# Kernel optimization log

Hardware: AMD Instinct MI355X
Metric: run time of the kernel (lower is better)

Reference implementation:

```python
import jax, jax.numpy as jnp
import numpy as np

B, N_SIDE, S = 64, 40, 512
N = N_SIDE * N_SIDE          # 1600 grid points (fl_feature_dims [1,40,40])
EMB = 10                     # embedding_dim
GDIM = 8                     # lie('homography').dim
WIDTH = 128
C1 = 20                      # first-layer output channels


def _embed(x, emb_dim):
    # sinusoidal embedding of each scalar coordinate: [..., D] -> [..., D*emb_dim]
    freqs = 2.0 ** jnp.arange(emb_dim // 2, dtype=x.dtype)
    ang = x[..., None] * freqs                       # [..., D, emb/2]
    e = jnp.concatenate([jnp.sin(ang), jnp.cos(ang)], axis=-1)  # [..., D, emb]
    return e.reshape(x.shape[:-1] + (x.shape[-1] * emb_dim,))


def _glorot(key, shape):
    fan_in = shape[0]
    return jax.random.normal(key, shape, dtype=jnp.float32) / np.sqrt(fan_in)


def setup_inputs() -> dict:
    key = jax.random.key(0)
    ks = jax.random.split(key, 16)
    inp = {
        'data':   jax.random.normal(ks[0], (B, N, 1), dtype=jnp.float32),
        'v0':     jax.random.normal(ks[1], (S, GDIM), dtype=jnp.float32),
        'v_last': jax.random.normal(ks[2], (S, GDIM), dtype=jnp.float32),
        # FirstLayer filter MLP: 2*EMB -> 20 -> 20 -> 1*C1
        'fl_w1': _glorot(ks[3], (2 * EMB, 20)), 'fl_b1': jnp.zeros((20,), jnp.float32),
        'fl_w2': _glorot(ks[4], (20, 20)),      'fl_b2': jnp.zeros((20,), jnp.float32),
        'fl_w3': _glorot(ks[5], (20, C1)),      'fl_b3': jnp.zeros((C1,), jnp.float32),
        # Hidden FilterMLP: EMB*GDIM=80 -> WIDTH -> C1*WIDTH
        's_w1': _glorot(ks[6], (EMB * GDIM, WIDTH)), 's_b1': jnp.zeros((WIDTH,), jnp.float32),
        's_w2': _glorot(ks[7], (WIDTH, C1 * WIDTH)), 's_b2': jnp.zeros((C1 * WIDTH,), jnp.float32),
        'fc1_w': _glorot(ks[8], (WIDTH, WIDTH)), 'fc1_b': jnp.zeros((WIDTH,), jnp.float32),
        'fc2_w': _glorot(ks[9], (WIDTH, WIDTH)), 'fc2_b': jnp.zeros((WIDTH,), jnp.float32),
        'pool_w': _glorot(ks[10], (WIDTH, 10)),  'pool_b': jnp.zeros((10,), jnp.float32),
    }
    return inp


def reference(data, v0, v_last, fl_w1, fl_b1, fl_w2, fl_b2, fl_w3, fl_b3,
              s_w1, s_b1, s_w2, s_b2, fc1_w, fc1_b, fc2_w, fc2_b, pool_w, pool_b):
    silu = jax.nn.silu
    # pixel grid in [-1,1]^2, homogeneous coords [N,3]
    lin = jnp.linspace(-1.0, 1.0, N_SIDE, dtype=data.dtype)
    xx, yy = jnp.meshgrid(lin, lin, indexing='ij')
    coords = jnp.stack([xx.ravel(), yy.ravel()], axis=-1)           # [N,2]
    xh = jnp.concatenate([coords, jnp.ones((N, 1), data.dtype)], -1)  # [N,3]
    # homography matrices: identity + small perturbation from 8 group params
    pert = jnp.concatenate([0.1 * v_last, jnp.zeros((S, 1), data.dtype)], -1).reshape(S, 3, 3)
    H = jnp.eye(3, dtype=data.dtype) + pert                          # [S,3,3]
    y = jnp.einsum('sij,nj->sni', H, xh)                             # [S,N,3]
    t = y[..., :2] / y[..., 2:3]                                     # projective action [S,N,2]
    # continuous-kernel first layer: filters generated by MLP on embedded coords
    e1 = _embed(t, EMB)                                              # [S,N,20]
    h = silu(e1 @ fl_w1 + fl_b1)
    h = silu(h @ fl_w2 + fl_b2)
    filt1 = h @ fl_w3 + fl_b3                                        # [S,N,C1]
    z = jnp.einsum('bn,sno->bso', data[:, :, 0], filt1) / N          # [B,S,C1]
    z = silu(z)
    # hidden FilterMLP on group samples v0 -> per-sample filters [S,C1,WIDTH]
    v0e = _embed(v0, EMB)                                            # [S,80]
    h2 = silu(v0e @ s_w1 + s_b1)                                     # [S,WIDTH]
    filt2 = (h2 @ s_w2 + s_b2).reshape(S, C1, WIDTH)
    # (1/S) * sum over group-sample and channel axes of broadcast product
    z = jnp.einsum('bsc,scw->bw', z, filt2) / S                      # [B,WIDTH]
    z = silu(z @ fc1_w + fc1_b) + z
    z = silu(z @ fc2_w + fc2_b) + z
    return z @ pool_w + pool_b                                       # [B,10]
```

## Files before the change

### kernel.cpp

```cpp
#include <hip/hip_runtime.h>

#define N_PTS 1600
#define NSIDE 40
#define SNUM  512
#define BNUM  64
#define C1D   20
#define WID   128

typedef _Float16 h8  __attribute__((ext_vector_type(8)));
typedef _Float16 h4  __attribute__((ext_vector_type(4)));
typedef __fp16   h2v __attribute__((ext_vector_type(2)));
typedef float    f4  __attribute__((ext_vector_type(4)));

__device__ __forceinline__ float silu_f(float x){
    return x * __builtin_amdgcn_rcpf(1.f + __expf(-x));
}
__device__ __forceinline__ void fma4(float4& a, float s, const float4 w){
    a.x += s*w.x; a.y += s*w.y; a.z += s*w.z; a.w += s*w.w;
}

__device__ __forceinline__ void embed_coord(
    int n, float hA, float hB, float hC, float h6, float h7, float h8c,
    h2v e5[5])
{
    const int i = n / NSIDE;
    const int j = n - i * NSIDE;
    const float x = -1.f + (float)i * (2.f/39.f);
    const float y = -1.f + (float)j * (2.f/39.f);
    const float yc = hA*x + hB*y + hC;
    const float y2 = h6*x + h7*y + h8c;
    const float tc = yc * __builtin_amdgcn_rcpf(y2);
    float e[10];
    float sv, cv;
    __sincosf(tc, &sv, &cv);
    #pragma unroll
    for (int k = 0; k < 5; k++) {
        e[k] = sv; e[5+k] = cv;
        const float ns = 2.f*sv*cv, nc = 1.f - 2.f*sv*sv; sv = ns; cv = nc;
    }
    #pragma unroll
    for (int k = 0; k < 5; k++)
        e5[k] = __builtin_amdgcn_cvt_pkrtz(e[2*k], e[2*k+1]);
}

#define ASTRIDE 40

__global__ __launch_bounds__(512, 6) void kaf_fused(
    const float* __restrict__ data, const float* __restrict__ v0,
    const float* __restrict__ v_last,
    const float* __restrict__ s_w1, const float* __restrict__ s_b1,
    const float* __restrict__ s_w2, const float* __restrict__ s_b2,
    const float* __restrict__ w1, const float* __restrict__ b1,
    const float* __restrict__ w2, const float* __restrict__ b2,
    const float* __restrict__ w3, const float* __restrict__ b3,
    _Float16* __restrict__ dataA, float* __restrict__ f2g,
    float* __restrict__ out2g, _Float16* __restrict__ filtG)
{
    const int t  = threadIdx.x;
    const int bx = blockIdx.x;

    __shared__ __align__(16) unsigned char smem[27008];

    if (bx >= 1024) {
        if (bx == 1689) {
            for (int v = t; v < 8192; v += 512) out2g[v] = 0.f;
            return;
        }
        if (bx >= 1664) {
            const int o  = (bx - 1664) * 512 + t;
            const int L  = o & 63, cm = o >> 6;
            const int mt = cm & 3, ch = cm >> 2;
            const int b  = mt * 16 + (L & 15);
            const int nb = ch * 32 + (L >> 4) * 8;
            const float* src = data + b * N_PTS + nb;
            h8 v;
            #pragma unroll
            for (int j = 0; j < 8; j++) v[j] = (_Float16)src[j];
            *(h8*)(dataA + (size_t)o * 8) = v;
            return;
        }
        const int bxe = bx - 1024;
        const int st  = bxe / 10, ct = bxe - st * 10;
        const int s0  = st * 8;
        float* h2t = (float*)smem;
        float* svt = (float*)(smem + 6144);

        if (t < 64) {
            const int ss = t >> 3, d = t & 7;
            const float val = v0[(s0 + ss) * 8 + d];
            float sv, cv;
            __sincosf(val, &sv, &cv);
            #pragma unroll
            for (int k = 0; k < 5; k++) {
                svt[(ss*8 + d)*10 + k]     = sv;
                svt[(ss*8 + d)*10 + 5 + k] = cv;
                const float ns = 2.f * sv * cv;
                const float nc = 1.f - 2.f * sv * sv;
                sv = ns; cv = nc;
            }
        }
        __syncthreads();

        {
            const int j  = t & 127;
            const int sh = t >> 7;
            const float bias1 = s_b1[j];
            float h0 = bias1, h1 = bias1;
            for (int d = 0; d < 8; d++) {
                #pragma unroll
                for (int kk = 0; kk < 10; kk++) {
                    const float wv = s_w1[(d * 10 + kk) * WID + j];
                    h0 += svt[((sh*2    )*8 + d)*10 + kk] * wv;
                    h1 += svt[((sh*2 + 1)*8 + d)*10 + kk] * wv;
                }
            }
            h2t[j*12 + sh*2    ] = silu_f(h0);
            h2t[j*12 + sh*2 + 1] = silu_f(h1);
        }
        __syncthreads();

        const int col = ct * 256 + (t & 255);
        const int g   = t >> 8;
        float4 acc = make_float4(0.f, 0.f, 0.f, 0.f);
        #pragma unroll 4
        for (int i = 0; i < 128; i++) {
            const float wv = s_w2[i * 2560 + col];
            const float4 hh = *(const float4*)&h2t[i*12 + g*4];
            fma4(acc, wv, hh);
        }
        const float bias = s_b2[col];
        const float* af = (const float*)&acc;
        #pragma unroll
        for (int u = 0; u < 4; u++)
            f2g[(s0 + g*4 + u) * 2560 + col] = af[u] + bias;
        return;
    }

    const int s    = bx & 511;
    const int half = bx >> 9;
    const int nb0  = half * 800;
    const int lane = t & 63;
    const int w    = t >> 6;
    const int q    = lane >> 4;
    const int l15  = lane & 15;
    const int ep   = lane >> 1;
    const int ec   = lane & 1;
    const int erow = w*16 + ep + ((ep >> 4) * 112);

    _Float16* act  = (_Float16*)smem;
    _Float16* wlds = (_Float16*)(smem + 20480);
    float*    blds = (float*)   (smem + 26624);

    {
        const float* wsrc[3] = { w1, w2, w3 };
        const float* bsrc[3] = { b1, b2, b3 };
        for (int v = t; v < 3072; v += 512) {
            const int l = v >> 10, rem = v & 1023;
            const int cout = rem >> 5, cin = rem & 31;
            float x = 0.f;
            if (cout < 20 && cin < 20) x = wsrc[l][cin * 20 + cout];
            wlds[v] = (_Float16)x;
        }
        if (t < 96) {
            const int l = t >> 5, cout = t & 31;
            blds[t] = (cout < 20) ? bsrc[l][cout] : 0.f;
        }
    }

    float Hm[9];
    #pragma unroll
    for (int k = 0; k < 9; k++) Hm[k] = (k == 0 || k == 4 || k == 8) ? 1.f : 0.f;
    #pragma unroll
    for (int k = 0; k < 8; k++) Hm[k] += 0.1f * v_last[s*8 + k];
    const float hA = ec ? Hm[3] : Hm[0];
    const float hB = ec ? Hm[4] : Hm[1];
    const float hC = ec ? Hm[5] : Hm[2];

    if (ec == 0) {
        unsigned long long* pz = (unsigned long long*)(act + erow*ASTRIDE + 20);
        pz[0] = 0ull; pz[1] = 0ull; pz[2] = 0ull;
    }

    __syncthreads();

    _Float16* fgs = filtG + (size_t)(half*512 + s) * 16000;

    for (int base = 0; base < 800; base += 256) {
        const int tn = min(256, 800 - base);

        if (erow < tn) {
            h2v e5[5];
            embed_coord(nb0 + base + erow, hA, hB, hC, Hm[6], Hm[7], Hm[8], e5);
            #pragma unroll
            for (int k = 0; k < 5; k++)
                *(h2v*)(act + erow*ASTRIDE + ec*10 + 2*k) = e5[k];
        }

        const int nmt = tn >> 4;
        #pragma unroll
        for (int l = 0; l < 3; l++) {
            const h8 wf0 = *(const h8*)(wlds + ((l*2+0)*16 + l15) * 32 + q*8);
            const h8 wf1 = *(const h8*)(wlds + ((l*2+1)*16 + l15) * 32 + q*8);
            const float b0 = blds[(l*2+0)*16 + l15];
            const float b1 = blds[(l*2+1)*16 + l15];
            const f4 zero4 = (f4)(0.f);
            for (int mt = w; mt < nmt; mt += 8) {
                const int r0 = mt * 16;
                const h8 af = *(const h8*)(act + (r0 + l15)*ASTRIDE + q*8);
                f4 D0 = __builtin_amdgcn_mfma_f32_16x16x32_f16(af, wf0, zero4, 0, 0, 0);
                f4 D1 = __builtin_amdgcn_mfma_f32_16x16x32_f16(af, wf1, zero4, 0, 0, 0);
                if (l < 2) {
                    #pragma unroll
                    for (int r = 0; r < 4; r++) {
                        const int p = r0 + q*4 + r;
                        act[p*ASTRIDE + l15] = (_Float16)silu_f(D0[r] + b0);
                        if (l15 < 4)
                            act[p*ASTRIDE + 16 + l15] = (_Float16)silu_f(D1[r] + b1);
                    }
                } else {
                    h4 p0, p1;
                    #pragma unroll
                    for (int r = 0; r < 4; r++) {
                        p0[r] = (_Float16)(D0[r] + b0);
                        p1[r] = (_Float16)(D1[r] + b1);
                    }
                    *(h4*)(fgs + l15*800 + base + r0 + q*4) = p0;
                    if (l15 < 4)
                        *(h4*)(fgs + (16 + l15)*800 + base + r0 + q*4) = p1;
                }
            }
        }
    }
}

__global__ __launch_bounds__(256, 6) void kz_gemm(
    const _Float16* __restrict__ dataA, const _Float16* __restrict__ filtG,
    float* __restrict__ zpart)
{
    const int s    = blockIdx.x & 511;
    const int half = blockIdx.x >> 9;
    const int t    = threadIdx.x;
    const int lane = t & 63;
    const int w    = t >> 6;
    const int q    = lane >> 4;
    const int l15  = lane & 15;

    __shared__ __align__(16) float red[4 * 64 * 21];

    const _Float16* fgs = filtG + (size_t)(half*512 + s) * 16000;
    const int r1row = (l15 < 4) ? (16 + l15) : 0;

    f4 zacc[4][2];
    #pragma unroll
    for (int mt = 0; mt < 4; mt++) { zacc[mt][0] = (f4)(0.f); zacc[mt][1] = (f4)(0.f); }

    #pragma unroll 2
    for (int kc = w; kc < 25; kc += 4) {
        const h8 bf0 = *(const h8*)(fgs + l15  *800 + kc*32 + q*8);
        const h8 bf1 = *(const h8*)(fgs + r1row*800 + kc*32 + q*8);
        const int gchunk = half*25 + kc;
        #pragma unroll
        for (int mt = 0; mt < 4; mt++) {
            const h8 afz = *(const h8*)(dataA + ((size_t)(gchunk*4 + mt)*64 + lane)*8);
            zacc[mt][0] = __builtin_amdgcn_mfma_f32_16x16x32_f16(afz, bf0, zacc[mt][0], 0, 0, 0);
            zacc[mt][1] = __builtin_amdgcn_mfma_f32_16x16x32_f16(afz, bf1, zacc[mt][1], 0, 0, 0);
        }
    }

    #pragma unroll
    for (int mt = 0; mt < 4; mt++) {
        #pragma unroll
        for (int r = 0; r < 4; r++) {
            const int b = mt*16 + q*4 + r;
            red[(w*64 + b)*21 + l15] = zacc[mt][0][r];
            if (l15 < 4) red[(w*64 + b)*21 + 16 + l15] = zacc[mt][1][r];
        }
    }
    __syncthreads();
    for (int v = t; v < 1280; v += 256) {
        const int c = v >> 6, b = v & 63;
        const float sum = red[(      b)*21 + c] + red[( 64 + b)*21 + c]
                        + red[(128 + b)*21 + c] + red[(192 + b)*21 + c];
        zpart[(half*512 + s)*1280 + v] = sum;
    }
}

__global__ __launch_bounds__(256) void k2_contract(
    const float* __restrict__ zg, const float* __restrict__ f2g,
    float* __restrict__ out2g)
{
    const int blk = blockIdx.x;
    const int sg  = blk >> 2;
    const int wq  = blk & 3;
    const int s0  = sg * 4;
    const int w0  = wq * 32;
    const int t   = threadIdx.x;
    __shared__ __align__(16) float zl[4*1280];
    __shared__ __align__(16) float fl[4*20*32];
    #pragma unroll
    for (int sp = 0; sp < 4; sp++) {
        const int srow = (s0 + sp) * 1280;
        for (int r = t; r < 1280; r += 256) {
            const float a0 = zg[srow + r];
            const float a1 = zg[512*1280 + srow + r];
            zl[sp*1280 + r] = silu_f((a0 + a1) * (1.f / (float)N_PTS));
        }
        for (int u = t; u < 640; u += 256) {
            const int c = u >> 5, ww = u & 31;
            fl[sp*640 + u] = f2g[(s0 + sp)*2560 + c*128 + w0 + ww];
        }
    }
    __syncthreads();
    const int ww = t & 31, bh = t >> 5;
    float4 acc[2];
    acc[0] = make_float4(0.f, 0.f, 0.f, 0.f);
    acc[1] = make_float4(0.f, 0.f, 0.f, 0.f);
    #pragma unroll 4
    for (int sc = 0; sc < 80; sc++) {
        const float f = fl[sc * 32 + ww];
        const float4* zz = (const float4*)&zl[sc * 64 + bh * 8];
        fma4(acc[0], f, zz[0]);
        fma4(acc[1], f, zz[1]);
    }
    const float* af = (const float*)acc;
    #pragma unroll
    for (int idx = 0; idx < 8; idx++) {
        const int b = bh * 8 + idx;
        atomicAdd(&out2g[b * 128 + w0 + ww], af[idx]);
    }
}

__global__ __launch_bounds__(128) void k3_tail(
    const float* __restrict__ out2g,
    const float* __restrict__ fc1w, const float* __restrict__ fc1b,
    const float* __restrict__ fc2w, const float* __restrict__ fc2b,
    const float* __restrict__ pw,   const float* __restrict__ pb,
    float* __restrict__ out)
{
    const int b = blockIdx.x, t = threadIdx.x;
    __shared__ float zb[128], r1[128], r2[128];
    zb[t] = out2g[b * 128 + t] * (1.f / (float)SNUM);
    __syncthreads();
    float a = fc1b[t];
    #pragma unroll 8
    for (int i = 0; i < 128; i++) a += zb[i] * fc1w[i * 128 + t];
    r1[t] = silu_f(a) + zb[t];
    __syncthreads();
    a = fc2b[t];
    #pragma unroll 8
    for (int i = 0; i < 128; i++) a += r1[i] * fc2w[i * 128 + t];
    r2[t] = silu_f(a) + r1[t];
    __syncthreads();
    if (t < 10) {
        float o = pb[t];
        #pragma unroll 8
        for (int i = 0; i < 128; i++) o += r2[i] * pw[i * 10 + t];
        out[b * 10 + t] = o;
    }
}

extern "C" void kernel_launch(void* const* d_in, const int* in_sizes, int n_in,
                              void* d_out, int out_size, void* d_ws, size_t ws_size,
                              hipStream_t stream) {
    const float* data   = (const float*)d_in[0];
    const float* v0     = (const float*)d_in[1];
    const float* v_last = (const float*)d_in[2];
    const float* fl_w1  = (const float*)d_in[3];
    const float* fl_b1  = (const float*)d_in[4];
    const float* fl_w2  = (const float*)d_in[5];
    const float* fl_b2  = (const float*)d_in[6];
    const float* fl_w3  = (const float*)d_in[7];
    const float* fl_b3  = (const float*)d_in[8];
    const float* s_w1   = (const float*)d_in[9];
    const float* s_b1   = (const float*)d_in[10];
    const float* s_w2   = (const float*)d_in[11];
    const float* s_b2   = (const float*)d_in[12];
    const float* fc1_w  = (const float*)d_in[13];
    const float* fc1_b  = (const float*)d_in[14];
    const float* fc2_w  = (const float*)d_in[15];
    const float* fc2_b  = (const float*)d_in[16];
    const float* pool_w = (const float*)d_in[17];
    const float* pool_b = (const float*)d_in[18];
    float* out = (float*)d_out;

    float* ws        = (float*)d_ws;
    _Float16* dataA  = (_Float16*)ws;
    float* zpart  = ws    + 51200;
    float* f2g    = zpart + 1310720;
    float* out2g  = f2g   + 1310720;
    _Float16* filtG = (_Float16*)(out2g + 8192);

    kaf_fused  <<<1690, 512, 0, stream>>>(data, v0, v_last,
                                          s_w1, s_b1, s_w2, s_b2,
                                          fl_w1, fl_b1, fl_w2, fl_b2, fl_w3, fl_b3,
                                          dataA, f2g, out2g, filtG);
    kz_gemm    <<<1024, 256, 0, stream>>>(dataA, filtG, zpart);
    k2_contract<<<512, 256, 0, stream>>>(zpart, f2g, out2g);
    k3_tail    <<<64, 128, 0, stream>>>(out2g, fc1_w, fc1_b, fc2_w, fc2_b,
                                        pool_w, pool_b, out);
}
```

Before: 168.3 us.

## Move hidden filter MLP onto MFMA with a separate prep kernel

Adds a prep kernel that computes the v0 embedding and first hidden layer with fp16 MFMA, transposes s_w2 to fp16, converts data, and zeroes the output accumulator. The s_w2 GEMM blocks inside the fused kernel now use MFMA tiles instead of scalar FMA loops. The first-layer MLP loop is restructured with transposed MFMA operands so each lane writes vectorized h4 activations, and occupancy hints are raised. It costs an extra kernel launch and lowers precision for the hidden filter path to fp16.

Measured after the change: 164.2 us, median of 2. 2.4% less time.

```diff
diff --git a/kernel.cpp b/kernel.cpp
--- a/kernel.cpp
+++ b/kernel.cpp
@@ -17,6 +17,77 @@
 }
 __device__ __forceinline__ void fma4(float4& a, float s, const float4 w){
     a.x += s*w.x; a.y += s*w.y; a.z += s*w.z; a.w += s*w.w;
+}
+
+__global__ __launch_bounds__(512) void kp_prep(
+    const float* __restrict__ data, const float* __restrict__ v0,
+    const float* __restrict__ s_w1, const float* __restrict__ s_b1,
+    const float* __restrict__ s_w2,
+    _Float16* __restrict__ dataA, _Float16* __restrict__ s_w2hT,
+    _Float16* __restrict__ h2G, float* __restrict__ out2g)
+{
+    const int t = threadIdx.x, bx = blockIdx.x;
+    if (bx >= 32) {
+        if (bx < 112) {
+            const int u  = (bx - 32) * 512 + t;
+            const int n  = u >> 4, k0 = (u & 15) * 8;
+            h8 v;
+            #pragma unroll
+            for (int j = 0; j < 8; j++) v[j] = (_Float16)s_w2[(k0 + j) * 2560 + n];
+            *(h8*)(s_w2hT + n * 128 + k0) = v;
+        } else if (bx < 137) {
+            const int o  = (bx - 112) * 512 + t;
+            const int L  = o & 63, cm = o >> 6;
+            const int mt = cm & 3, ch = cm >> 2;
+            const int b  = mt * 16 + (L & 15);
+            const int nb = ch * 32 + (L >> 4) * 8;
+            const float* src = data + b * N_PTS + nb;
+            h8 v;
+            #pragma unroll
+            for (int j = 0; j < 8; j++) v[j] = (_Float16)src[j];
+            *(h8*)(dataA + (size_t)o * 8) = v;
+        } else {
+            for (int v = t; v < 8192; v += 512) out2g[v] = 0.f;
+        }
+        return;
+    }
+    const int s0 = bx * 16;
+    __shared__ __align__(16) _Float16 w1T[12288];
+    __shared__ __align__(16) _Float16 svtA[1536];
+    for (int u = t; u < 12288; u += 512) {
+        const int j = u / 96, k = u - j * 96;
+        w1T[u] = (_Float16)((k < 80) ? s_w1[k * 128 + j] : 0.f);
+    }
+    for (int u = t; u < 1536; u += 512) svtA[u] = (_Float16)0.f;
+    __syncthreads();
+    if (t < 128) {
+        const int ss = t >> 3, d = t & 7;
+        const float val = v0[(s0 + ss) * 8 + d];
+        float sv, cv;
+        __sincosf(val, &sv, &cv);
+        #pragma unroll
+        for (int k = 0; k < 5; k++) {
+            svtA[ss * 96 + d * 10 + k]     = (_Float16)sv;
+            svtA[ss * 96 + d * 10 + 5 + k] = (_Float16)cv;
+            const float ns = 2.f * sv * cv, nc = 1.f - 2.f * sv * sv;
+            sv = ns; cv = nc;
+        }
+    }
+    __syncthreads();
+    const int lane = t & 63, w = t >> 6;
+    const int q = lane >> 4, l15 = lane & 15;
+    const f4 zero4 = (f4)(0.f);
+    f4 D = zero4;
+    #pragma unroll
+    for (int kc = 0; kc < 3; kc++) {
+        const h8 af = *(const h8*)(svtA + l15 * 96 + kc * 32 + q * 8);
+        const h8 bf = *(const h8*)(w1T + (w * 16 + l15) * 96 + kc * 32 + q * 8);
+        D = __builtin_amdgcn_mfma_f32_16x16x32_f16(af, bf, D, 0, 0, 0);
+    }
+    const float b = s_b1[w * 16 + l15];
+    #pragma unroll
+    for (int r = 0; r < 4; r++)
+        h2G[(s0 + q * 4 + r) * 128 + w * 16 + l15] = (_Float16)silu_f(D[r] + b);
 }
 
 __device__ __forceinline__ void embed_coord(
@@ -45,104 +116,50 @@
 
 #define ASTRIDE 40
 
-__global__ __launch_bounds__(512, 6) void kaf_fused(
-    const float* __restrict__ data, const float* __restrict__ v0,
+__global__ __launch_bounds__(512, 8) void kaf_fused(
     const float* __restrict__ v_last,
-    const float* __restrict__ s_w1, const float* __restrict__ s_b1,
-    const float* __restrict__ s_w2, const float* __restrict__ s_b2,
     const float* __restrict__ w1, const float* __restrict__ b1,
     const float* __restrict__ w2, const float* __restrict__ b2,
     const float* __restrict__ w3, const float* __restrict__ b3,
-    _Float16* __restrict__ dataA, float* __restrict__ f2g,
-    float* __restrict__ out2g, _Float16* __restrict__ filtG)
+    const float* __restrict__ s_b2,
+    const _Float16* __restrict__ s_w2hT, const _Float16* __restrict__ h2G,
+    float* __restrict__ f2g, _Float16* __restrict__ filtG)
 {
     const int t  = threadIdx.x;
     const int bx = blockIdx.x;
+    const int lane = t & 63, w = t >> 6;
+    const int q = lane >> 4, l15 = lane & 15;
+    const f4 zero4 = (f4)(0.f);
 
     __shared__ __align__(16) unsigned char smem[27008];
 
     if (bx >= 1024) {
-        if (bx == 1689) {
-            for (int v = t; v < 8192; v += 512) out2g[v] = 0.f;
-            return;
-        }
-        if (bx >= 1664) {
-            const int o  = (bx - 1664) * 512 + t;
-            const int L  = o & 63, cm = o >> 6;
-            const int mt = cm & 3, ch = cm >> 2;
-            const int b  = mt * 16 + (L & 15);
-            const int nb = ch * 32 + (L >> 4) * 8;
-            const float* src = data + b * N_PTS + nb;
-            h8 v;
+        const int bxe = bx - 1024;
+        const int mt = bxe / 10, ct = bxe - mt * 10;
+        h8 af[4];
+        #pragma unroll
+        for (int kc = 0; kc < 4; kc++)
+            af[kc] = *(const h8*)(h2G + (mt * 16 + l15) * 128 + kc * 32 + q * 8);
+        #pragma unroll
+        for (int i = 0; i < 2; i++) {
+            const int n0 = ct * 256 + (w + 8 * i) * 16;
+            f4 D = zero4;
             #pragma unroll
-            for (int j = 0; j < 8; j++) v[j] = (_Float16)src[j];
-            *(h8*)(dataA + (size_t)o * 8) = v;
-            return;
-        }
-        const int bxe = bx - 1024;
-        const int st  = bxe / 10, ct = bxe - st * 10;
-        const int s0  = st * 8;
-        float* h2t = (float*)smem;
-        float* svt = (float*)(smem + 6144);
-
-        if (t < 64) {
-            const int ss = t >> 3, d = t & 7;
-            const float val = v0[(s0 + ss) * 8 + d];
-            float sv, cv;
-            __sincosf(val, &sv, &cv);
+            for (int kc = 0; kc < 4; kc++) {
+                const h8 bf = *(const h8*)(s_w2hT + (n0 + l15) * 128 + kc * 32 + q * 8);
+                D = __builtin_amdgcn_mfma_f32_16x16x32_f16(af[kc], bf, D, 0, 0, 0);
+            }
+            const float bb = s_b2[n0 + l15];
             #pragma unroll
-            for (int k = 0; k < 5; k++) {
-                svt[(ss*8 + d)*10 + k]     = sv;
-                svt[(ss*8 + d)*10 + 5 + k] = cv;
-                const float ns = 2.f * sv * cv;
-                const float nc = 1.f - 2.f * sv * sv;
-                sv = ns; cv = nc;
-            }
-        }
-        __syncthreads();
-
-        {
-            const int j  = t & 127;
-            const int sh = t >> 7;
-            const float bias1 = s_b1[j];
-            float h0 = bias1, h1 = bias1;
-            for (int d = 0; d < 8; d++) {
-                #pragma unroll
-                for (int kk = 0; kk < 10; kk++) {
-                    const float wv = s_w1[(d * 10 + kk) * WID + j];
-                    h0 += svt[((sh*2    )*8 + d)*10 + kk] * wv;
-                    h1 += svt[((sh*2 + 1)*8 + d)*10 + kk] * wv;
-                }
-            }
-            h2t[j*12 + sh*2    ] = silu_f(h0);
-            h2t[j*12 + sh*2 + 1] = silu_f(h1);
-        }
-        __syncthreads();
-
-        const int col = ct * 256 + (t & 255);
-        const int g   = t >> 8;
-        float4 acc = make_float4(0.f, 0.f, 0.f, 0.f);
-        #pragma unroll 4
-        for (int i = 0; i < 128; i++) {
-            const float wv = s_w2[i * 2560 + col];
-            const float4 hh = *(const float4*)&h2t[i*12 + g*4];
-            fma4(acc, wv, hh);
-        }
-        const float bias = s_b2[col];
-        const float* af = (const float*)&acc;
-        #pragma unroll
-        for (int u = 0; u < 4; u++)
-            f2g[(s0 + g*4 + u) * 2560 + col] = af[u] + bias;
+            for (int r = 0; r < 4; r++)
+                f2g[(mt * 16 + q * 4 + r) * 2560 + n0 + l15] = D[r] + bb;
+        }
         return;
     }
 
     const int s    = bx & 511;
     const int half = bx >> 9;
     const int nb0  = half * 800;
-    const int lane = t & 63;
-    const int w    = t >> 6;
-    const int q    = lane >> 4;
-    const int l15  = lane & 15;
     const int ep   = lane >> 1;
     const int ec   = lane & 1;
     const int erow = w*16 + ep + ((ep >> 4) * 112);
@@ -196,38 +213,75 @@
                 *(h2v*)(act + erow*ASTRIDE + ec*10 + 2*k) = e5[k];
         }
 
-        const int nmt = tn >> 4;
-        #pragma unroll
-        for (int l = 0; l < 3; l++) {
+        const int nmt  = tn >> 4;
+        const bool hasA = w < nmt;
+        const bool hasB = (w + 8) < nmt;
+        const int rA = w * 16, rB = (w + 8) * 16;
+
+        #pragma unroll
+        for (int l = 0; l < 2; l++) {
             const h8 wf0 = *(const h8*)(wlds + ((l*2+0)*16 + l15) * 32 + q*8);
             const h8 wf1 = *(const h8*)(wlds + ((l*2+1)*16 + l15) * 32 + q*8);
-            const float b0 = blds[(l*2+0)*16 + l15];
-            const float b1 = blds[(l*2+1)*16 + l15];
-            const f4 zero4 = (f4)(0.f);
+            const float4 bD0 = *(const float4*)&blds[l*32 + q*4];
+            const float4 bD1 = *(const float4*)&blds[l*32 + 16 + q*4];
+            if (hasA) {
+                const h8 af = *(const h8*)(act + (rA + l15)*ASTRIDE + q*8);
+                const f4 D0 = __builtin_amdgcn_mfma_f32_16x16x32_f16(wf0, af, zero4, 0, 0, 0);
+                const f4 D1 = __builtin_amdgcn_mfma_f32_16x16x32_f16(wf1, af, zero4, 0, 0, 0);
+                h4 pv;
+                pv[0] = (_Float16)silu_f(D0[0] + bD0.x);
+                pv[1] = (_Float16)silu_f(D0[1] + bD0.y);
+                pv[2] = (_Float16)silu_f(D0[2] + bD0.z);
+                pv[3] = (_Float16)silu_f(D0[3] + bD0.w);
+                *(h4*)(act + (rA + l15)*ASTRIDE + q*4) = pv;
+                if (q == 0) {
+                    h4 pu;
+                    pu[0] = (_Float16)silu_f(D1[0] + bD1.x);
+                    pu[1] = (_Float16)silu_f(D1[1] + bD1.y);
+                    pu[2] = (_Float16)silu_f(D1[2] + bD1.z);
+                    pu[3] = (_Float16)silu_f(D1[3] + bD1.w);
+                    *(h4*)(act + (rA + l15)*ASTRIDE + 16) = pu;
+                }
+            }
+            if (hasB) {
+                const h8 af = *(const h8*)(act + (rB + l15)*ASTRIDE + q*8);
+                const f4 D0 = __builtin_amdgcn_mfma_f32_16x16x32_f16(wf0, af, zero4, 0, 0, 0);
+                const f4 D1 = __builtin_amdgcn_mfma_f32_16x16x32_f16(wf1, af, zero4, 0, 0, 0);
+                h4 pv;
+                pv[0] = (_Float16)silu_f(D0[0] + bD0.x);
+                pv[1] = (_Float16)silu_f(D0[1] + bD0.y);
+                pv[2] = (_Float16)silu_f(D0[2] + bD0.z);
+                pv[3] = (_Float16)silu_f(D0[3] + bD0.w);
+                *(h4*)(act + (rB + l15)*ASTRIDE + q*4) = pv;
+                if (q == 0) {
+                    h4 pu;
+                    pu[0] = (_Float16)silu_f(D1[0] + bD1.x);
+                    pu[1] = (_Float16)silu_f(D1[1] + bD1.y);
+                    pu[2] = (_Float16)silu_f(D1[2] + bD1.z);
+                    pu[3] = (_Float16)silu_f(D1[3] + bD1.w);
+                    *(h4*)(act + (rB + l15)*ASTRIDE + 16) = pu;
+                }
+            }
+        }
+        {
+            const h8 wf0 = *(const h8*)(wlds + (64 + l15) * 32 + q*8);
+            const h8 wf1 = *(const h8*)(wlds + (80 + l15) * 32 + q*8);
+            const float b20 = blds[64 + l15];
+            const float b21 = blds[80 + l15];
             for (int mt = w; mt < nmt; mt += 8) {
                 const int r0 = mt * 16;
                 const h8 af = *(const h8*)(act + (r0 + l15)*ASTRIDE + q*8);
                 f4 D0 = __builtin_amdgcn_mfma_f32_16x16x32_f16(af, wf0, zero4, 0, 0, 0);
                 f4 D1 = __builtin_amdgcn_mfma_f32_16x16x32_f16(af, wf1, zero4, 0, 0, 0);
-                if (l < 2) {
-                    #pragma unroll
-                    for (int r = 0; r < 4; r++) {
-                        const int p = r0 + q*4 + r;
-                        act[p*ASTRIDE + l15] = (_Float16)silu_f(D0[r] + b0);
-                        if (l15 < 4)
-                            act[p*ASTRIDE + 16 + l15] = (_Float16)silu_f(D1[r] + b1);
-                    }
-                } else {
-                    h4 p0, p1;
-                    #pragma unroll
-                    for (int r = 0; r < 4; r++) {
-                        p0[r] = (_Float16)(D0[r] + b0);
-                        p1[r] = (_Float16)(D1[r] + b1);
-                    }
-                    *(h4*)(fgs + l15*800 + base + r0 + q*4) = p0;
-                    if (l15 < 4)
-                        *(h4*)(fgs + (16 + l15)*800 + base + r0 + q*4) = p1;
+                h4 p0, p1;
+                #pragma unroll
+                for (int r = 0; r < 4; r++) {
+                    p0[r] = (_Float16)(D0[r] + b20);
+                    p1[r] = (_Float16)(D1[r] + b21);
                 }
+                *(h4*)(fgs + l15*800 + base + r0 + q*4) = p0;
+                if (l15 < 4)
+                    *(h4*)(fgs + (16 + l15)*800 + base + r0 + q*4) = p1;
             }
         }
     }
@@ -388,12 +442,15 @@
     float* zpart  = ws    + 51200;
     float* f2g    = zpart + 1310720;
     float* out2g  = f2g   + 1310720;
-    _Float16* filtG = (_Float16*)(out2g + 8192);
-
-    kaf_fused  <<<1690, 512, 0, stream>>>(data, v0, v_last,
-                                          s_w1, s_b1, s_w2, s_b2,
+    _Float16* s_w2hT = (_Float16*)(out2g + 8192);
+    _Float16* h2G    = (_Float16*)(out2g + 8192 + 163840);
+    _Float16* filtG  = (_Float16*)(out2g + 8192 + 163840 + 32768);
+
+    kp_prep    <<<138, 512, 0, stream>>>(data, v0, s_w1, s_b1, s_w2,
+                                         dataA, s_w2hT, h2G, out2g);
+    kaf_fused  <<<1344, 512, 0, stream>>>(v_last,
                                           fl_w1, fl_b1, fl_w2, fl_b2, fl_w3, fl_b3,
-                                          dataA, f2g, out2g, filtG);
+                                          s_b2, s_w2hT, h2G, f2g, filtG);
     kz_gemm    <<<1024, 256, 0, stream>>>(dataA, filtG, zpart);
     k2_contract<<<512, 256, 0, stream>>>(zpart, f2g, out2g);
     k3_tail    <<<64, 128, 0, stream>>>(out2g, fc1_w, fc1_b, fc2_w, fc2_b,
```
